# Performance work log

Measured on AMD Instinct MI355X. Metric: run time of the kernel, lower is better.

## Reference

```python
import jax, jax.numpy as jnp
import numpy as np

N, E, NFEAT, HID, HEADS, NCLASS = 100000, 1600000, 256, 64, 1, 32


def gat_conv(x, src, dst, W, a_src, a_dst, b, H, C, concat):
    n = x.shape[0]
    h = (x @ W).reshape(n, H, C)                      # [N,H,C]
    a_s = (h * a_src).sum(-1)                          # [N,H]
    a_d = (h * a_dst).sum(-1)                          # [N,H]
    e = jax.nn.leaky_relu(a_s[src] + a_d[dst], 0.2)    # [E,H]
    emax = jax.ops.segment_max(e, dst, num_segments=n)
    emax = jnp.where(jnp.isfinite(emax), emax, 0.0)
    ex = jnp.exp(e - emax[dst])
    denom = jax.ops.segment_sum(ex, dst, num_segments=n)
    alpha = ex / (denom[dst] + 1e-16)                  # segment softmax over in-edges of dst
    msg = h[src] * alpha[:, :, None]                   # [E,H,C]
    out = jax.ops.segment_sum(msg, dst, num_segments=n)
    out = out.reshape(n, H * C) if concat else out.mean(axis=1)
    return out + b


def setup_inputs() -> dict:
    key = jax.random.key(0)
    ks = jax.random.split(key, 14)
    x = jax.random.normal(ks[0], (N, NFEAT), dtype=jnp.float32)
    edge_index = jax.random.randint(ks[1], (2, E), 0, N, dtype=jnp.int64)
    s = 0.05
    return {
        'x': x, 'edge_index': edge_index,
        'W1': jax.random.normal(ks[2], (NFEAT, HEADS * HID), jnp.float32) * s,
        'as1': jax.random.normal(ks[3], (HEADS, HID), jnp.float32) * s,
        'ad1': jax.random.normal(ks[4], (HEADS, HID), jnp.float32) * s,
        'b1': jnp.zeros((HEADS * HID,), jnp.float32),
        'W2': jax.random.normal(ks[5], (HEADS * HID, HEADS * HID), jnp.float32) * s,
        'as2': jax.random.normal(ks[6], (HEADS, HID), jnp.float32) * s,
        'ad2': jax.random.normal(ks[7], (HEADS, HID), jnp.float32) * s,
        'b2': jnp.zeros((HEADS * HID,), jnp.float32),
        'W3': jax.random.normal(ks[8], (HEADS * HID, HEADS * NCLASS), jnp.float32) * s,
        'as3': jax.random.normal(ks[9], (HEADS, NCLASS), jnp.float32) * s,
        'ad3': jax.random.normal(ks[10], (HEADS, NCLASS), jnp.float32) * s,
        'b3': jnp.zeros((NCLASS,), jnp.float32),
    }


def reference(x, edge_index, W1, as1, ad1, b1, W2, as2, ad2, b2, W3, as3, ad3, b3):
    # add self loops (PyG GATConv add_self_loops=True)
    loop = jnp.arange(N, dtype=edge_index.dtype)
    src = jnp.concatenate([edge_index[0], loop])
    dst = jnp.concatenate([edge_index[1], loop])
    out = jax.nn.leaky_relu(gat_conv(x, src, dst, W1, as1, ad1, b1, HEADS, HID, True), 0.01)
    out = jax.nn.leaky_relu(gat_conv(out, src, dst, W2, as2, ad2, b2, HEADS, HID, True), 0.01)
    out = gat_conv(out, src, dst, W3, as3, ad3, b3, HEADS, NCLASS, False)
    return out
```

## Files before the change

kernel.cpp:

```cpp
#include <hip/hip_runtime.h>

#define NN 100000
#define NE 1600000
#define NF 256
#define HD 64
#define NC 32

#define BKS 8
#define NBK ((NN + 255) >> 8)
#define CHUNK 4096
#define NBLK ((NE + CHUNK - 1) / CHUNK)

__device__ __forceinline__ float lrelu02(float x) { return fmaxf(x, 0.2f * x); }


__global__ __launch_bounds__(256) void bucket_hist(const int* __restrict__ dst, int* __restrict__ gcnt) {
    __shared__ int hist[NBK];
    int tid = threadIdx.x;
    for (int i = tid; i < NBK; i += 256) hist[i] = 0;
    __syncthreads();
    int base = blockIdx.x * CHUNK;
    #pragma unroll
    for (int k = 0; k < CHUNK / 256; k++) {
        int i = base + k * 256 + tid;
        if (i < NE) atomicAdd(&hist[dst[i] >> BKS], 1);
    }
    __syncthreads();
    for (int i = tid; i < NBK; i += 256) if (hist[i]) atomicAdd(&gcnt[i], hist[i]);
}

__global__ void bucket_scan(const int* __restrict__ gcnt, int* __restrict__ gbase, int* __restrict__ gcur) {
    __shared__ int sh[512];
    int tid = threadIdx.x;
    int v = (tid < NBK) ? gcnt[tid] : 0;
    sh[tid] = v;
    __syncthreads();
    for (int d = 1; d < 512; d <<= 1) {
        int t = (tid >= d) ? sh[tid - d] : 0;
        __syncthreads();
        sh[tid] += t;
        __syncthreads();
    }
    if (tid < NBK) { int ex = sh[tid] - v; gbase[tid] = ex; gcur[tid] = ex; }
}

__global__ __launch_bounds__(256) void bin_edges(const int* __restrict__ src, const int* __restrict__ dst,
                                                 int* __restrict__ gcur, int2* __restrict__ ebuf) {
    __shared__ int hist[NBK];
    __shared__ int excl[NBK];
    __shared__ int runbase[NBK];
    __shared__ int ssum[256];
    __shared__ int2 sorted[CHUNK];
    int tid = threadIdx.x;
    int base = blockIdx.x * CHUNK;
    int n = NE - base; if (n > CHUNK) n = CHUNK;

    for (int i = tid; i < NBK; i += 256) hist[i] = 0;
    __syncthreads();

    int2 ed[CHUNK / 256];
    int bk[CHUNK / 256];
    #pragma unroll
    for (int k = 0; k < CHUNK / 256; k++) {
        int i = base + k * 256 + tid;
        if (i < NE) {
            ed[k] = make_int2(src[i], dst[i]);
            bk[k] = ed[k].y >> BKS;
            atomicAdd(&hist[bk[k]], 1);
        } else bk[k] = -1;
    }
    __syncthreads();
    int h0 = (2 * tid < NBK) ? hist[2 * tid] : 0;
    int h1 = (2 * tid + 1 < NBK) ? hist[2 * tid + 1] : 0;
    ssum[tid] = h0 + h1;
    __syncthreads();
    for (int d = 1; d < 256; d <<= 1) {
        int t = (tid >= d) ? ssum[tid - d] : 0;
        __syncthreads();
        ssum[tid] += t;
        __syncthreads();
    }
    int pref = ssum[tid] - (h0 + h1);
    if (2 * tid < NBK) excl[2 * tid] = pref;
    if (2 * tid + 1 < NBK) excl[2 * tid + 1] = pref + h0;
    for (int b = tid; b < NBK; b += 256) {
        int c = hist[b];
        runbase[b] = c ? atomicAdd(&gcur[b], c) : 0;
    }
    __syncthreads();
    #pragma unroll
    for (int k = 0; k < CHUNK / 256; k++) {
        if (bk[k] >= 0) {
            int r = atomicAdd(&excl[bk[k]], 1);
            sorted[r] = ed[k];
        }
    }
    __syncthreads();
    for (int i = tid; i < n; i += 256) {
        int2 e = sorted[i];
        int b = e.y >> BKS;
        int local_rank = i - (excl[b] - hist[b]);
        ebuf[runbase[b] + local_rank] = e;
    }
}

__global__ __launch_bounds__(256) void bucket_csr(const int2* __restrict__ ebuf, const int* __restrict__ gbase,
                                                  const int* __restrict__ gcnt,
                                                  int* __restrict__ offs, int* __restrict__ csr) {
    __shared__ int hist[256], cur[256], ssum[256];
    int b = blockIdx.x, tid = threadIdx.x;
    int ebeg = gbase[b], cnt = gcnt[b];
    int node0 = b << BKS;
    hist[tid] = 0;
    __syncthreads();
    for (int i = ebeg + tid; i < ebeg + cnt; i += 256)
        atomicAdd(&hist[ebuf[i].y & 255], 1);
    __syncthreads();
    int v = hist[tid];
    ssum[tid] = v;
    __syncthreads();
    for (int d = 1; d < 256; d <<= 1) {
        int t = (tid >= d) ? ssum[tid - d] : 0;
        __syncthreads();
        ssum[tid] += t;
        __syncthreads();
    }
    int ex = ebeg + ssum[tid] - v;
    cur[tid] = ex;
    int nnode = NN - node0; if (nnode > 256) nnode = 256;
    if (tid < nnode) offs[node0 + tid] = ex;
    if (b == NBK - 1 && tid == nnode - 1) offs[NN] = ebeg + cnt;
    __syncthreads();
    for (int i = ebeg + tid; i < ebeg + cnt; i += 256) {
        int2 e = ebuf[i];
        int pos = atomicAdd(&cur[e.y & 255], 1);
        csr[pos] = e.x;
    }
}


template <int CIN, int COUT, int COLT, int NPT>
__global__ __launch_bounds__(256) void rb_gemm(const float* __restrict__ in, const float* __restrict__ W,
                                               const float* __restrict__ a_s, const float* __restrict__ a_d,
                                               float* __restrict__ h, float* __restrict__ asv,
                                               float* __restrict__ adv) {
    const int KC  = 64;
    const int BN  = (256 / COLT) * NPT;
    const int LDX = KC + 2;
    __shared__ float xs[BN * LDX];
    __shared__ float Wl[KC * COUT];
    int tid = threadIdx.x;
    int cg = tid % COLT;
    int ng = tid / COLT;
    int c0 = cg * 4;

    float4 acc[NPT];
    #pragma unroll
    for (int i = 0; i < NPT; i++) acc[i] = make_float4(0.f, 0.f, 0.f, 0.f);

    for (int k0 = 0; k0 < CIN; k0 += KC) {
        __syncthreads();
        #pragma unroll
        for (int r = 0; r < BN * KC / 4 / 256; r++) {
            int flat = r * 256 + tid;
            int n = flat >> 4;
            int q = flat & 15;
            int gn = blockIdx.x * BN + n;
            float4 v = make_float4(0.f, 0.f, 0.f, 0.f);
            if (gn < NN) v = *(const float4*)&in[(size_t)gn * CIN + k0 + q * 4];
            float* p = &xs[n * LDX + q * 4];
            *(float2*)p = make_float2(v.x, v.y);
            *(float2*)(p + 2) = make_float2(v.z, v.w);
        }
        #pragma unroll
        for (int r = 0; r < KC * COUT / 4 / 256; r++) {
            int flat = (r * 256 + tid) * 4;
            *(float4*)&Wl[flat] = *(const float4*)&W[(size_t)k0 * COUT + flat];
        }
        __syncthreads();
        #pragma unroll 4
        for (int k = 0; k < KC; k += 2) {
            float4 w0 = *(float4*)&Wl[k * COUT + c0];
            float4 w1 = *(float4*)&Wl[(k + 1) * COUT + c0];
            #pragma unroll
            for (int i = 0; i < NPT; i++) {
                float2 xv = *(float2*)&xs[(ng * NPT + i) * LDX + k];
                acc[i].x += xv.x * w0.x; acc[i].y += xv.x * w0.y;
                acc[i].z += xv.x * w0.z; acc[i].w += xv.x * w0.w;
                acc[i].x += xv.y * w1.x; acc[i].y += xv.y * w1.y;
                acc[i].z += xv.y * w1.z; acc[i].w += xv.y * w1.w;
            }
        }
    }
    float4 As4 = *(const float4*)&a_s[c0];
    float4 Ad4 = *(const float4*)&a_d[c0];
    #pragma unroll
    for (int i = 0; i < NPT; i++) {
        int n = blockIdx.x * BN + ng * NPT + i;
        if (n < NN) *(float4*)&h[(size_t)n * COUT + c0] = acc[i];
        float vs = acc[i].x * As4.x + acc[i].y * As4.y + acc[i].z * As4.z + acc[i].w * As4.w;
        float vd = acc[i].x * Ad4.x + acc[i].y * Ad4.y + acc[i].z * Ad4.z + acc[i].w * Ad4.w;
        #pragma unroll
        for (int off = 1; off < COLT; off <<= 1) { vs += __shfl_xor(vs, off); vd += __shfl_xor(vd, off); }
        if (cg == 0 && n < NN) { asv[n] = vs; adv[n] = vd; }
    }
}


template <int C, bool ACT>
__global__ __launch_bounds__(256) void gat_agg(const float* __restrict__ h, const float* __restrict__ asv,
                                               const float* __restrict__ adv, const int* __restrict__ offs,
                                               const int* __restrict__ csr,
                                               const float* __restrict__ bias, float* __restrict__ out) {
    const int LPR = C / 4;
    const int G = 64 / LPR;
    const float4* h4 = (const float4*)h;
    int lane = threadIdx.x & 63;
    int v = blockIdx.x * 4 + (threadIdx.x >> 6);
    int beg = offs[v], end = offs[v + 1];
    int g = lane / LPR, r = lane % LPR;
    float adv_v = adv[v];

    float4 acc = {0.f, 0.f, 0.f, 0.f};
    float dsum = 0.f;
    #pragma unroll 4
    for (int e = beg + g; e < end; e += G) {
        int s = csr[e];
        float ww = __expf(lrelu02(asv[s] + adv_v));
        float4 hv = h4[(size_t)s * LPR + r];
        dsum += ww;
        acc.x += ww * hv.x; acc.y += ww * hv.y; acc.z += ww * hv.z; acc.w += ww * hv.w;
    }
    #pragma unroll
    for (int off = LPR; off < 64; off <<= 1) {
        acc.x += __shfl_xor(acc.x, off);
        acc.y += __shfl_xor(acc.y, off);
        acc.z += __shfl_xor(acc.z, off);
        acc.w += __shfl_xor(acc.w, off);
        dsum += __shfl_xor(dsum, off);
    }
    if (g == 0) {
        float selfw = __expf(lrelu02(asv[v] + adv_v));
        float4 hs = h4[(size_t)v * LPR + r];
        acc.x += selfw * hs.x; acc.y += selfw * hs.y;
        acc.z += selfw * hs.z; acc.w += selfw * hs.w;
        dsum += selfw;
        float inv = 1.f / (dsum + 1e-16f);
        float4 bb = ((const float4*)bias)[r];
        float4 o;
        o.x = acc.x * inv + bb.x; o.y = acc.y * inv + bb.y;
        o.z = acc.z * inv + bb.z; o.w = acc.w * inv + bb.w;
        if (ACT) {
            o.x = fmaxf(o.x, 0.01f * o.x); o.y = fmaxf(o.y, 0.01f * o.y);
            o.z = fmaxf(o.z, 0.01f * o.z); o.w = fmaxf(o.w, 0.01f * o.w);
        }
        ((float4*)out)[(size_t)v * LPR + r] = o;
    }
}


extern "C" void kernel_launch(void* const* d_in, const int* in_sizes, int n_in,
                              void* d_out, int out_size, void* d_ws, size_t ws_size,
                              hipStream_t stream) {
    const float* x   = (const float*)d_in[0];
    const int*   ei  = (const int*)d_in[1];
    const float* W1  = (const float*)d_in[2];
    const float* as1 = (const float*)d_in[3];
    const float* ad1 = (const float*)d_in[4];
    const float* b1  = (const float*)d_in[5];
    const float* W2  = (const float*)d_in[6];
    const float* as2 = (const float*)d_in[7];
    const float* ad2 = (const float*)d_in[8];
    const float* b2  = (const float*)d_in[9];
    const float* W3  = (const float*)d_in[10];
    const float* as3 = (const float*)d_in[11];
    const float* ad3 = (const float*)d_in[12];
    const float* b3  = (const float*)d_in[13];
    float* out = (float*)d_out;

    const int* srcp = ei;
    const int* dstp = ei + NE;

    char* w = (char*)d_ws;
    float* h     = (float*)w;   w += sizeof(float) * (size_t)NN * HD;
    float* featB = (float*)w;   w += sizeof(float) * (size_t)NN * HD;
    float* asv   = (float*)w;   w += sizeof(float) * NN;
    float* advv  = (float*)w;   w += sizeof(float) * NN;
    int* offs    = (int*)w;     w += sizeof(int) * (NN + 1);
    int* csr     = (int*)w;     w += sizeof(int) * (size_t)NE;
    int2* ebuf   = (int2*)w;    w += sizeof(int2) * (size_t)NE;
    int* gcnt    = (int*)w;     w += sizeof(int) * NBK;
    int* gbase   = (int*)w;     w += sizeof(int) * NBK;
    int* gcur    = (int*)w;     w += sizeof(int) * NBK;

    const int GB = (NN + 127) / 128;

    hipMemsetAsync(gcnt, 0, sizeof(int) * NBK, stream);
    bucket_hist<<<NBLK, 256, 0, stream>>>(dstp, gcnt);
    bucket_scan<<<1, 512, 0, stream>>>(gcnt, gbase, gcur);
    bin_edges<<<NBLK, 256, 0, stream>>>(srcp, dstp, gcur, ebuf);
    bucket_csr<<<NBK, 256, 0, stream>>>(ebuf, gbase, gcnt, offs, csr);

    rb_gemm<NF, HD, 16, 8><<<GB, 256, 0, stream>>>(x, W1, as1, ad1, h, asv, advv);
    gat_agg<HD, true><<<NN / 4, 256, 0, stream>>>(h, asv, advv, offs, csr, b1, featB);

    rb_gemm<HD, HD, 16, 8><<<GB, 256, 0, stream>>>(featB, W2, as2, ad2, h, asv, advv);
    gat_agg<HD, true><<<NN / 4, 256, 0, stream>>>(h, asv, advv, offs, csr, b2, featB);

    rb_gemm<HD, NC, 8, 4><<<GB, 256, 0, stream>>>(featB, W3, as3, ad3, h, asv, advv);
    gat_agg<NC, false><<<NN / 4, 256, 0, stream>>>(h, asv, advv, offs, csr, b3, out);
}
```

Baseline: 500.0 us.

## Restructure feature GEMM with transposed x tile and 4x8 register blocking

```diff
diff --git a/kernel.cpp b/kernel.cpp
--- a/kernel.cpp
+++ b/kernel.cpp
@@ -139,69 +139,76 @@
 }
 
 
-template <int CIN, int COUT, int COLT, int NPT>
+template <int CIN, int COUT, int CG>
 __global__ __launch_bounds__(256) void rb_gemm(const float* __restrict__ in, const float* __restrict__ W,
                                                const float* __restrict__ a_s, const float* __restrict__ a_d,
                                                float* __restrict__ h, float* __restrict__ asv,
                                                float* __restrict__ adv) {
-    const int KC  = 64;
-    const int BN  = (256 / COLT) * NPT;
-    const int LDX = KC + 2;
-    __shared__ float xs[BN * LDX];
+    const int KC  = 32;
+    const int NG  = 256 / CG;
+    const int BN  = NG * 4;
+    const int BNP = BN + 4;
+    __shared__ float xsT[KC * BNP];
     __shared__ float Wl[KC * COUT];
     int tid = threadIdx.x;
-    int cg = tid % COLT;
-    int ng = tid / COLT;
-    int c0 = cg * 4;
-
-    float4 acc[NPT];
-    #pragma unroll
-    for (int i = 0; i < NPT; i++) acc[i] = make_float4(0.f, 0.f, 0.f, 0.f);
+    int cg = tid % CG;
+    int ng = tid / CG;
+    int c0 = cg * 8;
+    int n0base = blockIdx.x * BN;
+
+    float4 a0[4], a1[4];
+    #pragma unroll
+    for (int i = 0; i < 4; i++) { a0[i] = make_float4(0,0,0,0); a1[i] = make_float4(0,0,0,0); }
 
     for (int k0 = 0; k0 < CIN; k0 += KC) {
         __syncthreads();
+        const int XF4 = BN * KC / 4;
         #pragma unroll
-        for (int r = 0; r < BN * KC / 4 / 256; r++) {
-            int flat = r * 256 + tid;
-            int n = flat >> 4;
-            int q = flat & 15;
-            int gn = blockIdx.x * BN + n;
-            float4 v = make_float4(0.f, 0.f, 0.f, 0.f);
+        for (int f = tid; f < XF4; f += 256) {
+            int n = f >> 3;
+            int q = f & 7;
+            int gn = n0base + n;
+            float4 v = make_float4(0,0,0,0);
             if (gn < NN) v = *(const float4*)&in[(size_t)gn * CIN + k0 + q * 4];
-            float* p = &xs[n * LDX + q * 4];
-            *(float2*)p = make_float2(v.x, v.y);
-            *(float2*)(p + 2) = make_float2(v.z, v.w);
+            xsT[(q * 4 + 0) * BNP + n] = v.x;
+            xsT[(q * 4 + 1) * BNP + n] = v.y;
+            xsT[(q * 4 + 2) * BNP + n] = v.z;
+            xsT[(q * 4 + 3) * BNP + n] = v.w;
         }
         #pragma unroll
-        for (int r = 0; r < KC * COUT / 4 / 256; r++) {
-            int flat = (r * 256 + tid) * 4;
-            *(float4*)&Wl[flat] = *(const float4*)&W[(size_t)k0 * COUT + flat];
-        }
+        for (int f = tid; f < KC * COUT / 4; f += 256)
+            *(float4*)&Wl[f * 4] = *(const float4*)&W[(size_t)k0 * COUT + f * 4];
         __syncthreads();
         #pragma unroll 4
-        for (int k = 0; k < KC; k += 2) {
+        for (int k = 0; k < KC; k++) {
+            float4 xv = *(float4*)&xsT[k * BNP + ng * 4];
             float4 w0 = *(float4*)&Wl[k * COUT + c0];
-            float4 w1 = *(float4*)&Wl[(k + 1) * COUT + c0];
+            float4 w1 = *(float4*)&Wl[k * COUT + c0 + 4];
             #pragma unroll
-            for (int i = 0; i < NPT; i++) {
-                float2 xv = *(float2*)&xs[(ng * NPT + i) * LDX + k];
-                acc[i].x += xv.x * w0.x; acc[i].y += xv.x * w0.y;
-                acc[i].z += xv.x * w0.z; acc[i].w += xv.x * w0.w;
-                acc[i].x += xv.y * w1.x; acc[i].y += xv.y * w1.y;
-                acc[i].z += xv.y * w1.z; acc[i].w += xv.y * w1.w;
+            for (int i = 0; i < 4; i++) {
+                float xc = (i == 0) ? xv.x : (i == 1) ? xv.y : (i == 2) ? xv.z : xv.w;
+                a0[i].x += xc * w0.x; a0[i].y += xc * w0.y; a0[i].z += xc * w0.z; a0[i].w += xc * w0.w;
+                a1[i].x += xc * w1.x; a1[i].y += xc * w1.y; a1[i].z += xc * w1.z; a1[i].w += xc * w1.w;
             }
         }
     }
-    float4 As4 = *(const float4*)&a_s[c0];
-    float4 Ad4 = *(const float4*)&a_d[c0];
-    #pragma unroll
-    for (int i = 0; i < NPT; i++) {
-        int n = blockIdx.x * BN + ng * NPT + i;
-        if (n < NN) *(float4*)&h[(size_t)n * COUT + c0] = acc[i];
-        float vs = acc[i].x * As4.x + acc[i].y * As4.y + acc[i].z * As4.z + acc[i].w * As4.w;
-        float vd = acc[i].x * Ad4.x + acc[i].y * Ad4.y + acc[i].z * Ad4.z + acc[i].w * Ad4.w;
+    float4 As0 = *(const float4*)&a_s[c0];
+    float4 As1 = *(const float4*)&a_s[c0 + 4];
+    float4 Ad0 = *(const float4*)&a_d[c0];
+    float4 Ad1 = *(const float4*)&a_d[c0 + 4];
+    #pragma unroll
+    for (int i = 0; i < 4; i++) {
+        int n = n0base + ng * 4 + i;
+        if (n < NN) {
+            *(float4*)&h[(size_t)n * COUT + c0] = a0[i];
+            *(float4*)&h[(size_t)n * COUT + c0 + 4] = a1[i];
+        }
+        float vs = a0[i].x * As0.x + a0[i].y * As0.y + a0[i].z * As0.z + a0[i].w * As0.w
+                 + a1[i].x * As1.x + a1[i].y * As1.y + a1[i].z * As1.z + a1[i].w * As1.w;
+        float vd = a0[i].x * Ad0.x + a0[i].y * Ad0.y + a0[i].z * Ad0.z + a0[i].w * Ad0.w
+                 + a1[i].x * Ad1.x + a1[i].y * Ad1.y + a1[i].z * Ad1.z + a1[i].w * Ad1.w;
         #pragma unroll
-        for (int off = 1; off < COLT; off <<= 1) { vs += __shfl_xor(vs, off); vd += __shfl_xor(vd, off); }
+        for (int off = 1; off < CG; off <<= 1) { vs += __shfl_xor(vs, off); vd += __shfl_xor(vd, off); }
         if (cg == 0 && n < NN) { asv[n] = vs; adv[n] = vd; }
     }
 }
@@ -293,7 +300,8 @@
     int* gbase   = (int*)w;     w += sizeof(int) * NBK;
     int* gcur    = (int*)w;     w += sizeof(int) * NBK;
 
-    const int GB = (NN + 127) / 128;
+    const int GB64 = (NN + 127) / 128;
+    const int GB32 = (NN + 255) / 256;
 
     hipMemsetAsync(gcnt, 0, sizeof(int) * NBK, stream);
     bucket_hist<<<NBLK, 256, 0, stream>>>(dstp, gcnt);
@@ -301,12 +309,12 @@
     bin_edges<<<NBLK, 256, 0, stream>>>(srcp, dstp, gcur, ebuf);
     bucket_csr<<<NBK, 256, 0, stream>>>(ebuf, gbase, gcnt, offs, csr);
 
-    rb_gemm<NF, HD, 16, 8><<<GB, 256, 0, stream>>>(x, W1, as1, ad1, h, asv, advv);
+    rb_gemm<NF, HD, 8><<<GB64, 256, 0, stream>>>(x, W1, as1, ad1, h, asv, advv);
     gat_agg<HD, true><<<NN / 4, 256, 0, stream>>>(h, asv, advv, offs, csr, b1, featB);
 
-    rb_gemm<HD, HD, 16, 8><<<GB, 256, 0, stream>>>(featB, W2, as2, ad2, h, asv, advv);
+    rb_gemm<HD, HD, 8><<<GB64, 256, 0, stream>>>(featB, W2, as2, ad2, h, asv, advv);
     gat_agg<HD, true><<<NN / 4, 256, 0, stream>>>(h, asv, advv, offs, csr, b2, featB);
 
-    rb_gemm<HD, NC, 8, 4><<<GB, 256, 0, stream>>>(featB, W3, as3, ad3, h, asv, advv);
+    rb_gemm<HD, NC, 4><<<GB32, 256, 0, stream>>>(featB, W3, as3, ad3, h, asv, advv);
     gat_agg<NC, false><<<NN / 4, 256, 0, stream>>>(h, asv, advv, offs, csr, b3, out);
 }
```

Result: faster. 476.8 us (-4.6%).
